# Kernel optimization log

Hardware: AMD Instinct MI355X
Metric: run time of the kernel (lower is better)

Reference implementation:

```python
import jax, jax.numpy as jnp
import numpy as np

N = 50000          # nodes
E = 800000         # edges (avg degree 16)
FEATS = [96, 96, 96, 48]


def setup_inputs() -> dict:
    key = jax.random.key(0)
    ks = jax.random.split(key, 10)
    x = jax.random.normal(ks[0], (N, FEATS[0]), dtype=jnp.float32)
    edge_index = jax.random.randint(ks[1], (2, E), 0, N, dtype=jnp.int64)
    d = {"x": x, "edge_index": edge_index}
    i = 2
    for l in range(3):
        s = 1.0 / np.sqrt(FEATS[l])
        d[f"Wl{l}"] = jax.random.uniform(ks[i], (FEATS[l], FEATS[l + 1]), jnp.float32, -s, s); i += 1
        d[f"Wr{l}"] = jax.random.uniform(ks[i], (FEATS[l], FEATS[l + 1]), jnp.float32, -s, s); i += 1
        d[f"b{l}"] = jnp.zeros((FEATS[l + 1],), jnp.float32)
    return d


def _sage_layer(h, src, dst, Wl, Wr, b, n):
    # PyG SAGEConv (aggr='mean', root_weight=True, normalize=False):
    # out_i = W_l @ mean_{j in N(i)} h_j + W_r @ h_i + b
    msg = h[src]                                                   # [E, F] gather
    ssum = jax.ops.segment_sum(msg, dst, num_segments=n)           # [N, F] scatter-add
    cnt = jax.ops.segment_sum(jnp.ones((src.shape[0], 1), h.dtype), dst, num_segments=n)
    mean = ssum / jnp.maximum(cnt, 1.0)
    return mean @ Wl + h @ Wr + b


def reference(x, edge_index, Wl0, Wr0, b0, Wl1, Wr1, b1, Wl2, Wr2, b2):
    src, dst = edge_index[0], edge_index[1]
    n = x.shape[0]
    # block = SAGEConv -> ReLU -> dropout(identity in eval)
    h = jax.nn.relu(_sage_layer(x, src, dst, Wl0, Wr0, b0, n))
    h = jax.nn.relu(_sage_layer(h, src, dst, Wl1, Wr1, b1, n))
    h = jax.nn.relu(_sage_layer(h, src, dst, Wl2, Wr2, b2, n))
    return h
```

## Files before the change

### kernel.cpp

```cpp
#include <hip/hip_runtime.h>


#define NNODES 50000
#define ZROW   50000
#define NEDGES 800000
#define CAP    64
#define LSTR   72
#define NBKT   512
#define BKSZ   98
#define NBKB   511
#define EBA    400
#define EPBA   2000
#define SEGC   20
#define CVT_N8 600000
#define CB 1172
#define WTN 46080
#define WB 90

typedef __attribute__((ext_vector_type(8))) short bf16x8;
typedef __attribute__((ext_vector_type(4))) float f32x4;

__device__ inline unsigned short f2bf(float f) {
    unsigned int u = __float_as_uint(f);
    unsigned int r = (u + 0x7fffu + ((u >> 16) & 1u)) >> 16;
    return (unsigned short)r;
}
__device__ inline float bf2f_lo(unsigned int u) { return __uint_as_float(u << 16); }
__device__ inline float bf2f_hi(unsigned int u) { return __uint_as_float(u & 0xffff0000u); }

__global__ __launch_bounds__(512) void build_a(
        const int* __restrict__ src, const int* __restrict__ dst,
        unsigned int* __restrict__ region, unsigned char* __restrict__ cnta,
        const float* __restrict__ x, unsigned short* __restrict__ h0b,
        const float* __restrict__ Wl0, const float* __restrict__ Wr0,
        const float* __restrict__ Wl1, const float* __restrict__ Wr1,
        const float* __restrict__ Wl2, const float* __restrict__ Wr2,
        unsigned short* __restrict__ WT0, unsigned short* __restrict__ WT1,
        unsigned short* __restrict__ WT2l, unsigned short* __restrict__ WT2r) {
    int b = blockIdx.x;
    if (b < EBA) {
        __shared__ int hist[NBKT];
        const int t = threadIdx.x;
        for (int k = t; k < NBKT; k += 512) hist[k] = 0;
        __syncthreads();
        const int e0 = b * EPBA;
        for (int i = t; i < EPBA; i += 512) {
            int d = dst[e0 + i];
            int s = src[e0 + i];
            unsigned int bk = (unsigned int)d / 98u;
            unsigned int rel = (unsigned int)d - bk * 98u;
            unsigned int val = (rel << 16) | (unsigned int)s;
            int r = atomicAdd(&hist[bk], 1);
            if (r < SEGC) region[((size_t)b * NBKT + bk) * SEGC + r] = val;
        }
        __syncthreads();
        for (int k = t; k < NBKT; k += 512)
            cnta[(size_t)k * EBA + b] = (unsigned char)min(hist[k], SEGC);
    } else if (b < EBA + CB) {
        long long t = (long long)(b - EBA) * 512 + threadIdx.x;
        if (t < CVT_N8) {
            const float4* p = reinterpret_cast<const float4*>(x + t * 8);
            float4 a = p[0], c = p[1];
            uint4 o;
            o.x = (unsigned)f2bf(a.x) | ((unsigned)f2bf(a.y) << 16);
            o.y = (unsigned)f2bf(a.z) | ((unsigned)f2bf(a.w) << 16);
            o.z = (unsigned)f2bf(c.x) | ((unsigned)f2bf(c.y) << 16);
            o.w = (unsigned)f2bf(c.z) | ((unsigned)f2bf(c.w) << 16);
            *reinterpret_cast<uint4*>(h0b + t * 8) = o;
        }
    } else if (b < EBA + CB + WB) {
        int t = (b - EBA - CB) * 512 + threadIdx.x;
        if (t >= WTN) return;
        if (t < 18432) {
            int u = t; int j = u / 192; int k = u - j * 192;
            float v = (k < 96) ? Wl0[k * 96 + j] : Wr0[(k - 96) * 96 + j];
            WT0[u] = f2bf(v);
        } else if (t < 36864) {
            int u = t - 18432; int j = u / 192; int k = u - j * 192;
            float v = (k < 96) ? Wl1[k * 96 + j] : Wr1[(k - 96) * 96 + j];
            WT1[u] = f2bf(v);
        } else if (t < 41472) {
            int u = t - 36864; int j = u / 96; int k = u - j * 96;
            WT2l[u] = f2bf(Wl2[k * 48 + j]);
        } else {
            int u = t - 41472; int j = u / 96; int k = u - j * 96;
            WT2r[u] = f2bf(Wr2[k * 48 + j]);
        }
    } else {
        int t = threadIdx.x;
        if (t < 12) {
            uint4 z = make_uint4(0, 0, 0, 0);
            *reinterpret_cast<uint4*>(h0b + (size_t)ZROW * 96 + t * 8) = z;
        }
    }
}

__global__ __launch_bounds__(512) void build_b(const unsigned int* __restrict__ region,
                                               const unsigned char* __restrict__ cnta,
                                               int* __restrict__ deg,
                                               unsigned short* __restrict__ colu) {
    __shared__ unsigned char cnt_l[EBA];
    __shared__ int deg_l[BKSZ];
    __shared__ __attribute__((aligned(16))) unsigned short colu_l[BKSZ * CAP];
    const int k = blockIdx.x;
    const int t = threadIdx.x;
    const int base_node = k * BKSZ;
    const int nn = min(BKSZ, NNODES - base_node);
    for (int i = t; i < EBA; i += 512) cnt_l[i] = cnta[(size_t)k * EBA + i];
    if (t < BKSZ) deg_l[t] = 0;
    __syncthreads();

    for (int cb = t; cb < EBA; cb += 512) {
        const int c = cnt_l[cb];
        const unsigned int* cell = region + ((size_t)cb * NBKT + k) * SEGC;
        for (int j = 0; j < c; j += 4) {
            uint4 q = *reinterpret_cast<const uint4*>(cell + j);
            unsigned int qq0 = q.x, qq1 = q.y, qq2 = q.z, qq3 = q.w;
            if (j + 0 < c) {
                int local = (int)(qq0 >> 16);
                int r = atomicAdd(&deg_l[local], 1);
                if (r < CAP) colu_l[local * CAP + r] = (unsigned short)(qq0 & 0xffffu);
            }
            if (j + 1 < c) {
                int local = (int)(qq1 >> 16);
                int r = atomicAdd(&deg_l[local], 1);
                if (r < CAP) colu_l[local * CAP + r] = (unsigned short)(qq1 & 0xffffu);
            }
            if (j + 2 < c) {
                int local = (int)(qq2 >> 16);
                int r = atomicAdd(&deg_l[local], 1);
                if (r < CAP) colu_l[local * CAP + r] = (unsigned short)(qq2 & 0xffffu);
            }
            if (j + 3 < c) {
                int local = (int)(qq3 >> 16);
                int r = atomicAdd(&deg_l[local], 1);
                if (r < CAP) colu_l[local * CAP + r] = (unsigned short)(qq3 & 0xffffu);
            }
        }
    }
    __syncthreads();

    for (int i = t; i < nn * (CAP / 8); i += 512) {
        *reinterpret_cast<uint4*>(colu + (size_t)base_node * CAP + i * 8) =
            *reinterpret_cast<const uint4*>(colu_l + i * 8);
    }
    if (t < nn) deg[base_node + t] = deg_l[t];
}

template <int NT, bool Y2EP>
__global__ __launch_bounds__(256) void fused_layer(
    const unsigned short* __restrict__ hb,
    const int* __restrict__ deg, const unsigned short* __restrict__ colu,
    const unsigned short* __restrict__ WT,
    const float* __restrict__ bias,
    unsigned short* __restrict__ out_bf,
    const unsigned short* __restrict__ WT2l,
    unsigned short* __restrict__ Y2b) {
    __shared__ unsigned short Asm[16][200];
    __shared__ unsigned short cols[16 * LSTR];
    const int i0 = blockIdx.x * 16;
    const int t = threadIdx.x;

    if (blockIdx.x == 0) {
        if (t < 12) {
            uint4 z = make_uint4(0, 0, 0, 0);
            *reinterpret_cast<uint4*>(out_bf + (size_t)ZROW * 96 + t * 8) = z;
        }
        if (Y2EP && t >= 16 && t < 22) {
            uint4 z = make_uint4(0, 0, 0, 0);
            *reinterpret_cast<uint4*>(Y2b + (size_t)ZROW * 48 + (t - 16) * 8) = z;
        }
    }

    {
        int u4 = t * 4;
        int node = u4 >> 6;
        int slot = u4 & 63;
        uint2 v = *reinterpret_cast<const uint2*>(colu + (size_t)(i0 + node) * CAP + slot);
        int d = deg[i0 + node];
        unsigned int s0 = (slot + 0 < d) ? (v.x & 0xffffu) : ZROW;
        unsigned int s1 = (slot + 1 < d) ? (v.x >> 16)     : ZROW;
        unsigned int s2 = (slot + 2 < d) ? (v.y & 0xffffu) : ZROW;
        unsigned int s3 = (slot + 3 < d) ? (v.y >> 16)     : ZROW;
        uint2 o;
        o.x = s0 | (s1 << 16);
        o.y = s2 | (s3 << 16);
        *reinterpret_cast<uint2*>(&cols[node * LSTR + slot]) = o;
    }
    __syncthreads();

    if (t < 192) {
        const int nl = t / 12;
        const int c = (t - nl * 12) * 8;
        const int d = deg[i0 + nl];
        const int d8 = d & ~7;
        const int pd4 = (d + 3) & ~3;
        float a0 = 0.f, a1 = 0.f, a2 = 0.f, a3 = 0.f, a4 = 0.f, a5 = 0.f, a6 = 0.f, a7 = 0.f;
        int j = 0;
        for (; j < d8; j += 8) {
            uint4 cu = *reinterpret_cast<const uint4*>(&cols[nl * LSTR + j]);
            int s0 = (int)(cu.x & 0xffffu), s1 = (int)(cu.x >> 16);
            int s2 = (int)(cu.y & 0xffffu), s3 = (int)(cu.y >> 16);
            int s4 = (int)(cu.z & 0xffffu), s5 = (int)(cu.z >> 16);
            int s6 = (int)(cu.w & 0xffffu), s7 = (int)(cu.w >> 16);
            uint4 u0 = *reinterpret_cast<const uint4*>(hb + (size_t)s0 * 96 + c);
            uint4 u1 = *reinterpret_cast<const uint4*>(hb + (size_t)s1 * 96 + c);
            uint4 u2 = *reinterpret_cast<const uint4*>(hb + (size_t)s2 * 96 + c);
            uint4 u3 = *reinterpret_cast<const uint4*>(hb + (size_t)s3 * 96 + c);
            uint4 u4 = *reinterpret_cast<const uint4*>(hb + (size_t)s4 * 96 + c);
            uint4 u5 = *reinterpret_cast<const uint4*>(hb + (size_t)s5 * 96 + c);
            uint4 u6 = *reinterpret_cast<const uint4*>(hb + (size_t)s6 * 96 + c);
            uint4 u7 = *reinterpret_cast<const uint4*>(hb + (size_t)s7 * 96 + c);
            a0 += bf2f_lo(u0.x) + bf2f_lo(u1.x) + bf2f_lo(u2.x) + bf2f_lo(u3.x)
                + bf2f_lo(u4.x) + bf2f_lo(u5.x) + bf2f_lo(u6.x) + bf2f_lo(u7.x);
            a1 += bf2f_hi(u0.x) + bf2f_hi(u1.x) + bf2f_hi(u2.x) + bf2f_hi(u3.x)
                + bf2f_hi(u4.x) + bf2f_hi(u5.x) + bf2f_hi(u6.x) + bf2f_hi(u7.x);
            a2 += bf2f_lo(u0.y) + bf2f_lo(u1.y) + bf2f_lo(u2.y) + bf2f_lo(u3.y)
                + bf2f_lo(u4.y) + bf2f_lo(u5.y) + bf2f_lo(u6.y) + bf2f_lo(u7.y);
            a3 += bf2f_hi(u0.y) + bf2f_hi(u1.y) + bf2f_hi(u2.y) + bf2f_hi(u3.y)
                + bf2f_hi(u4.y) + bf2f_hi(u5.y) + bf2f_hi(u6.y) + bf2f_hi(u7.y);
            a4 += bf2f_lo(u0.z) + bf2f_lo(u1.z) + bf2f_lo(u2.z) + bf2f_lo(u3.z)
                + bf2f_lo(u4.z) + bf2f_lo(u5.z) + bf2f_lo(u6.z) + bf2f_lo(u7.z);
            a5 += bf2f_hi(u0.z) + bf2f_hi(u1.z) + bf2f_hi(u2.z) + bf2f_hi(u3.z)
                + bf2f_hi(u4.z) + bf2f_hi(u5.z) + bf2f_hi(u6.z) + bf2f_hi(u7.z);
            a6 += bf2f_lo(u0.w) + bf2f_lo(u1.w) + bf2f_lo(u2.w) + bf2f_lo(u3.w)
                + bf2f_lo(u4.w) + bf2f_lo(u5.w) + bf2f_lo(u6.w) + bf2f_lo(u7.w);
            a7 += bf2f_hi(u0.w) + bf2f_hi(u1.w) + bf2f_hi(u2.w) + bf2f_hi(u3.w)
                + bf2f_hi(u4.w) + bf2f_hi(u5.w) + bf2f_hi(u6.w) + bf2f_hi(u7.w);
        }
        for (; j < pd4; j += 4) {
            uint2 cu = *reinterpret_cast<const uint2*>(&cols[nl * LSTR + j]);
            int s0 = (int)(cu.x & 0xffffu), s1 = (int)(cu.x >> 16);
            int s2 = (int)(cu.y & 0xffffu), s3 = (int)(cu.y >> 16);
            uint4 u0 = *reinterpret_cast<const uint4*>(hb + (size_t)s0 * 96 + c);
            uint4 u1 = *reinterpret_cast<const uint4*>(hb + (size_t)s1 * 96 + c);
            uint4 u2 = *reinterpret_cast<const uint4*>(hb + (size_t)s2 * 96 + c);
            uint4 u3 = *reinterpret_cast<const uint4*>(hb + (size_t)s3 * 96 + c);
            a0 += bf2f_lo(u0.x) + bf2f_lo(u1.x) + bf2f_lo(u2.x) + bf2f_lo(u3.x);
            a1 += bf2f_hi(u0.x) + bf2f_hi(u1.x) + bf2f_hi(u2.x) + bf2f_hi(u3.x);
            a2 += bf2f_lo(u0.y) + bf2f_lo(u1.y) + bf2f_lo(u2.y) + bf2f_lo(u3.y);
            a3 += bf2f_hi(u0.y) + bf2f_hi(u1.y) + bf2f_hi(u2.y) + bf2f_hi(u3.y);
            a4 += bf2f_lo(u0.z) + bf2f_lo(u1.z) + bf2f_lo(u2.z) + bf2f_lo(u3.z);
            a5 += bf2f_hi(u0.z) + bf2f_hi(u1.z) + bf2f_hi(u2.z) + bf2f_hi(u3.z);
            a6 += bf2f_lo(u0.w) + bf2f_lo(u1.w) + bf2f_lo(u2.w) + bf2f_lo(u3.w);
            a7 += bf2f_hi(u0.w) + bf2f_hi(u1.w) + bf2f_hi(u2.w) + bf2f_hi(u3.w);
        }
        float inv = (d > 0) ? 1.0f / (float)d : 0.0f;
        uint4 o;
        o.x = (unsigned)f2bf(a0 * inv) | ((unsigned)f2bf(a1 * inv) << 16);
        o.y = (unsigned)f2bf(a2 * inv) | ((unsigned)f2bf(a3 * inv) << 16);
        o.z = (unsigned)f2bf(a4 * inv) | ((unsigned)f2bf(a5 * inv) << 16);
        o.w = (unsigned)f2bf(a6 * inv) | ((unsigned)f2bf(a7 * inv) << 16);
        *reinterpret_cast<uint4*>(&Asm[nl][c]) = o;
    }
    __syncthreads();

    const int wave = t >> 6;
    const int lane = t & 63;
    const int m = lane & 15;
    const int kq = (lane >> 4) * 8;

    bf16x8 afr[6];
#pragma unroll
    for (int kk = 0; kk < 3; ++kk)
        afr[kk] = *reinterpret_cast<const bf16x8*>(&Asm[m][kq + kk * 32]);
    const unsigned short* hrow = hb + (size_t)(i0 + m) * 96 + kq;
#pragma unroll
    for (int kk = 0; kk < 3; ++kk)
        afr[3 + kk] = *reinterpret_cast<const bf16x8*>(hrow + kk * 32);

    if (Y2EP) __syncthreads();

    const int r0 = (lane >> 4) * 4;
    for (int nt = wave; nt < NT; nt += 4) {
        f32x4 acc = {0.f, 0.f, 0.f, 0.f};
        const unsigned short* wrow = WT + (size_t)(nt * 16 + m) * 192 + kq;
#pragma unroll
        for (int kk = 0; kk < 6; ++kk) {
            bf16x8 bfr = *reinterpret_cast<const bf16x8*>(wrow + kk * 32);
            acc = __builtin_amdgcn_mfma_f32_16x16x32_bf16(afr[kk], bfr, acc, 0, 0, 0);
        }
        int colj = nt * 16 + m;
        float bv = bias[colj];
#pragma unroll
        for (int r = 0; r < 4; ++r) {
            float v = fmaxf(acc[r] + bv, 0.0f);
            unsigned short hv = f2bf(v);
            out_bf[(size_t)(i0 + r0 + r) * (16 * NT) + colj] = hv;
            if (Y2EP) Asm[r0 + r][colj] = hv;
        }
    }

    if (Y2EP) {
        __syncthreads();
        if (wave < 3) {
            bf16x8 a2[3];
#pragma unroll
            for (int kk = 0; kk < 3; ++kk)
                a2[kk] = *reinterpret_cast<const bf16x8*>(&Asm[m][kq + kk * 32]);
            f32x4 acc = {0.f, 0.f, 0.f, 0.f};
            const unsigned short* wrow = WT2l + (size_t)(wave * 16 + m) * 96 + kq;
#pragma unroll
            for (int kk = 0; kk < 3; ++kk) {
                bf16x8 bfr = *reinterpret_cast<const bf16x8*>(wrow + kk * 32);
                acc = __builtin_amdgcn_mfma_f32_16x16x32_bf16(a2[kk], bfr, acc, 0, 0, 0);
            }
            int colj2 = wave * 16 + m;
#pragma unroll
            for (int r = 0; r < 4; ++r)
                Y2b[(size_t)(i0 + r0 + r) * 48 + colj2] = f2bf(acc[r]);
        }
    }
}

__global__ __launch_bounds__(256) void fused_final(
    const unsigned short* __restrict__ hb,
    const unsigned short* __restrict__ Y2b,
    const int* __restrict__ deg, const unsigned short* __restrict__ colu,
    const unsigned short* __restrict__ WT2r,
    const float* __restrict__ bias,
    float* __restrict__ out_f) {
    __shared__ float Msm[32][56];
    __shared__ unsigned short cols[32 * LSTR];
    const int i0 = blockIdx.x * 32;
    const int t = threadIdx.x;
    const int nn = min(32, NNODES - i0);

    {
        int node = t >> 3;
        int slot = (t & 7) * 8;
        uint4 v = *reinterpret_cast<const uint4*>(colu + (size_t)(i0 + node) * CAP + slot);
        int d = (node < nn) ? deg[i0 + node] : 0;
        unsigned int s0 = (slot + 0 < d) ? (v.x & 0xffffu) : ZROW;
        unsigned int s1 = (slot + 1 < d) ? (v.x >> 16)     : ZROW;
        unsigned int s2 = (slot + 2 < d) ? (v.y & 0xffffu) : ZROW;
        unsigned int s3 = (slot + 3 < d) ? (v.y >> 16)     : ZROW;
        unsigned int s4 = (slot + 4 < d) ? (v.z & 0xffffu) : ZROW;
        unsigned int s5 = (slot + 5 < d) ? (v.z >> 16)     : ZROW;
        unsigned int s6 = (slot + 6 < d) ? (v.w & 0xffffu) : ZROW;
        unsigned int s7 = (slot + 7 < d) ? (v.w >> 16)     : ZROW;
        uint4 o;
        o.x = s0 | (s1 << 16);
        o.y = s2 | (s3 << 16);
        o.z = s4 | (s5 << 16);
        o.w = s6 | (s7 << 16);
        *reinterpret_cast<uint4*>(&cols[node * LSTR + slot]) = o;
    }
    __syncthreads();

    if (t < 192) {
        const int nl = t / 6;
        const int c = (t - nl * 6) * 8;
        const int d = (nl < nn) ? deg[i0 + nl] : 0;
        const int d8 = d & ~7;
        const int pd4 = (d + 3) & ~3;
        float a0 = 0.f, a1 = 0.f, a2 = 0.f, a3 = 0.f, a4 = 0.f, a5 = 0.f, a6 = 0.f, a7 = 0.f;
        int j = 0;
        for (; j < d8; j += 8) {
            uint4 cu = *reinterpret_cast<const uint4*>(&cols[nl * LSTR + j]);
            int s0 = (int)(cu.x & 0xffffu), s1 = (int)(cu.x >> 16);
            int s2 = (int)(cu.y & 0xffffu), s3 = (int)(cu.y >> 16);
            int s4 = (int)(cu.z & 0xffffu), s5 = (int)(cu.z >> 16);
            int s6 = (int)(cu.w & 0xffffu), s7 = (int)(cu.w >> 16);
            uint4 u0 = *reinterpret_cast<const uint4*>(Y2b + (size_t)s0 * 48 + c);
            uint4 u1 = *reinterpret_cast<const uint4*>(Y2b + (size_t)s1 * 48 + c);
            uint4 u2 = *reinterpret_cast<const uint4*>(Y2b + (size_t)s2 * 48 + c);
            uint4 u3 = *reinterpret_cast<const uint4*>(Y2b + (size_t)s3 * 48 + c);
            uint4 u4 = *reinterpret_cast<const uint4*>(Y2b + (size_t)s4 * 48 + c);
            uint4 u5 = *reinterpret_cast<const uint4*>(Y2b + (size_t)s5 * 48 + c);
            uint4 u6 = *reinterpret_cast<const uint4*>(Y2b + (size_t)s6 * 48 + c);
            uint4 u7 = *reinterpret_cast<const uint4*>(Y2b + (size_t)s7 * 48 + c);
            a0 += bf2f_lo(u0.x) + bf2f_lo(u1.x) + bf2f_lo(u2.x) + bf2f_lo(u3.x)
                + bf2f_lo(u4.x) + bf2f_lo(u5.x) + bf2f_lo(u6.x) + bf2f_lo(u7.x);
            a1 += bf2f_hi(u0.x) + bf2f_hi(u1.x) + bf2f_hi(u2.x) + bf2f_hi(u3.x)
                + bf2f_hi(u4.x) + bf2f_hi(u5.x) + bf2f_hi(u6.x) + bf2f_hi(u7.x);
            a2 += bf2f_lo(u0.y) + bf2f_lo(u1.y) + bf2f_lo(u2.y) + bf2f_lo(u3.y)
                + bf2f_lo(u4.y) + bf2f_lo(u5.y) + bf2f_lo(u6.y) + bf2f_lo(u7.y);
            a3 += bf2f_hi(u0.y) + bf2f_hi(u1.y) + bf2f_hi(u2.y) + bf2f_hi(u3.y)
                + bf2f_hi(u4.y) + bf2f_hi(u5.y) + bf2f_hi(u6.y) + bf2f_hi(u7.y);
            a4 += bf2f_lo(u0.z) + bf2f_lo(u1.z) + bf2f_lo(u2.z) + bf2f_lo(u3.z)
                + bf2f_lo(u4.z) + bf2f_lo(u5.z) + bf2f_lo(u6.z) + bf2f_lo(u7.z);
            a5 += bf2f_hi(u0.z) + bf2f_hi(u1.z) + bf2f_hi(u2.z) + bf2f_hi(u3.z)
                + bf2f_hi(u4.z) + bf2f_hi(u5.z) + bf2f_hi(u6.z) + bf2f_hi(u7.z);
            a6 += bf2f_lo(u0.w) + bf2f_lo(u1.w) + bf2f_lo(u2.w) + bf2f_lo(u3.w)
                + bf2f_lo(u4.w) + bf2f_lo(u5.w) + bf2f_lo(u6.w) + bf2f_lo(u7.w);
            a7 += bf2f_hi(u0.w) + bf2f_hi(u1.w) + bf2f_hi(u2.w) + bf2f_hi(u3.w)
                + bf2f_hi(u4.w) + bf2f_hi(u5.w) + bf2f_hi(u6.w) + bf2f_hi(u7.w);
        }
        for (; j < pd4; j += 4) {
            uint2 cu = *reinterpret_cast<const uint2*>(&cols[nl * LSTR + j]);
            int s0 = (int)(cu.x & 0xffffu), s1 = (int)(cu.x >> 16);
            int s2 = (int)(cu.y & 0xffffu), s3 = (int)(cu.y >> 16);
            uint4 u0 = *reinterpret_cast<const uint4*>(Y2b + (size_t)s0 * 48 + c);
            uint4 u1 = *reinterpret_cast<const uint4*>(Y2b + (size_t)s1 * 48 + c);
            uint4 u2 = *reinterpret_cast<const uint4*>(Y2b + (size_t)s2 * 48 + c);
            uint4 u3 = *reinterpret_cast<const uint4*>(Y2b + (size_t)s3 * 48 + c);
            a0 += bf2f_lo(u0.x) + bf2f_lo(u1.x) + bf2f_lo(u2.x) + bf2f_lo(u3.x);
            a1 += bf2f_hi(u0.x) + bf2f_hi(u1.x) + bf2f_hi(u2.x) + bf2f_hi(u3.x);
            a2 += bf2f_lo(u0.y) + bf2f_lo(u1.y) + bf2f_lo(u2.y) + bf2f_lo(u3.y);
            a3 += bf2f_hi(u0.y) + bf2f_hi(u1.y) + bf2f_hi(u2.y) + bf2f_hi(u3.y);
            a4 += bf2f_lo(u0.z) + bf2f_lo(u1.z) + bf2f_lo(u2.z) + bf2f_lo(u3.z);
            a5 += bf2f_hi(u0.z) + bf2f_hi(u1.z) + bf2f_hi(u2.z) + bf2f_hi(u3.z);
            a6 += bf2f_lo(u0.w) + bf2f_lo(u1.w) + bf2f_lo(u2.w) + bf2f_lo(u3.w);
            a7 += bf2f_hi(u0.w) + bf2f_hi(u1.w) + bf2f_hi(u2.w) + bf2f_hi(u3.w);
        }
        float inv = (d > 0) ? 1.0f / (float)d : 0.0f;
        float4 o0 = make_float4(a0 * inv, a1 * inv, a2 * inv, a3 * inv);
        float4 o1 = make_float4(a4 * inv, a5 * inv, a6 * inv, a7 * inv);
        *reinterpret_cast<float4*>(&Msm[nl][c]) = o0;
        *reinterpret_cast<float4*>(&Msm[nl][c + 4]) = o1;
    }
    __syncthreads();

    const int wave = t >> 6;
    const int lane = t & 63;
    const int m = lane & 15;
    const int kq = (lane >> 4) * 8;
    const int r0 = (lane >> 4) * 4;

    for (int tt = wave; tt < 6; tt += 4) {
        const int rt = tt / 3;
        const int ct = tt - rt * 3;
        bf16x8 afr[3];
        const unsigned short* hrow = hb + (size_t)(i0 + rt * 16 + m) * 96 + kq;
#pragma unroll
        for (int kk = 0; kk < 3; ++kk)
            afr[kk] = *reinterpret_cast<const bf16x8*>(hrow + kk * 32);
        f32x4 acc = {0.f, 0.f, 0.f, 0.f};
        const unsigned short* wrow = WT2r + (size_t)(ct * 16 + m) * 96 + kq;
#pragma unroll
        for (int kk = 0; kk < 3; ++kk) {
            bf16x8 bfr = *reinterpret_cast<const bf16x8*>(wrow + kk * 32);
            acc = __builtin_amdgcn_mfma_f32_16x16x32_bf16(afr[kk], bfr, acc, 0, 0, 0);
        }
        int colj = ct * 16 + m;
        float bv = bias[colj];
#pragma unroll
        for (int r = 0; r < 4; ++r) {
            int row = rt * 16 + r0 + r;
            if (i0 + row < NNODES) {
                float v = fmaxf(acc[r] + Msm[row][colj] + bv, 0.0f);
                out_f[(size_t)(i0 + row) * 48 + colj] = v;
            }
        }
    }
}

extern "C" void kernel_launch(void* const* d_in, const int* in_sizes, int n_in,
                              void* d_out, int out_size, void* d_ws, size_t ws_size,
                              hipStream_t stream) {
    const float* x   = (const float*)d_in[0];
    const int*   ei  = (const int*)d_in[1];
    const float* Wl0 = (const float*)d_in[2];
    const float* Wr0 = (const float*)d_in[3];
    const float* b0  = (const float*)d_in[4];
    const float* Wl1 = (const float*)d_in[5];
    const float* Wr1 = (const float*)d_in[6];
    const float* b1  = (const float*)d_in[7];
    const float* Wl2 = (const float*)d_in[8];
    const float* Wr2 = (const float*)d_in[9];
    const float* b2  = (const float*)d_in[10];
    float* out = (float*)d_out;

    const int* src = ei;
    const int* dst = ei + NEDGES;

    char* p = (char*)d_ws;
    int* deg = (int*)p;                        p += (size_t)50176 * 4;
    unsigned short* colu = (unsigned short*)p; p += (size_t)50176 * CAP * 2;
    unsigned char* cnta = (unsigned char*)p;   p += (size_t)NBKT * EBA;
    unsigned short* WT0 = (unsigned short*)p;  p += 96 * 192 * 2;
    unsigned short* WT1 = (unsigned short*)p;  p += 96 * 192 * 2;
    unsigned short* WT2l = (unsigned short*)p; p += 48 * 96 * 2;
    unsigned short* WT2r = (unsigned short*)p; p += 48 * 96 * 2;
    unsigned short* h0b = (unsigned short*)p;  p += (size_t)(NNODES + 1) * 96 * 2 + 64;
    unsigned short* h1b = (unsigned short*)p;  p += (size_t)(NNODES + 1) * 96 * 2 + 64;
    unsigned short* h2b = (unsigned short*)p;  p += (size_t)(NNODES + 1) * 96 * 2 + 64;
    unsigned short* Y2b = (unsigned short*)p;  p += (size_t)(NNODES + 1) * 48 * 2 + 64;

    unsigned int* region = (unsigned int*)h1b;

    build_a<<<EBA + CB + WB + 1, 512, 0, stream>>>(
        src, dst, region, cnta, x, h0b,
        Wl0, Wr0, Wl1, Wr1, Wl2, Wr2, WT0, WT1, WT2l, WT2r);

    build_b<<<NBKB, 512, 0, stream>>>(region, cnta, deg, colu);

    const int LB = NNODES / 16;
    const int FB = (NNODES + 31) / 32;
    fused_layer<6, false><<<LB, 256, 0, stream>>>(h0b, deg, colu, WT0, b0, h1b,
                                                  nullptr, nullptr);
    fused_layer<6, true><<<LB, 256, 0, stream>>>(h1b, deg, colu, WT1, b1, h2b,
                                                 WT2l, Y2b);
    fused_final<<<FB, 256, 0, stream>>>(h2b, Y2b, deg, colu, WT2r, b2, out);
}
```

Baseline: 191.9 us.

## Fuse all stages into one cooperative persistent kernel with grid syncs

Replaces five separate launches (two graph build passes, two SAGE layers, final layer) with a single cooperative kernel of 512 blocks that runs each phase in turn, separated by grid-wide syncs. The layer phases use atomic tile counters for dynamic work distribution. Tiles grow from 16 to 32 rows (64 in the final layer) with 512 threads per block. The aim is to remove inter-kernel launch gaps and tail effects, at the cost of grid-sync overhead, lower occupancy constraints and a shared-memory footprint that is the union of all phases. A fallback to separate launches is kept in case the cooperative launch fails.

```diff
diff --git a/kernel.cpp b/kernel.cpp
--- a/kernel.cpp
+++ b/kernel.cpp
@@ -1,4 +1,7 @@
 #include <hip/hip_runtime.h>
+#include <hip/hip_cooperative_groups.h>
+
+namespace cg = cooperative_groups;
 
 
 #define NNODES 50000
@@ -9,13 +12,14 @@
 #define NBKT   512
 #define BKSZ   98
 #define NBKB   511
-#define EBA    400
-#define EPBA   2000
+#define EBA    512
+#define EPBA   1563
 #define SEGC   20
 #define CVT_N8 600000
-#define CB 1172
-#define WTN 46080
-#define WB 90
+#define WTN    46080
+#define NTILE_L 1563
+#define NTILE_F 782
+#define HROWS  50016
 
 typedef __attribute__((ext_vector_type(8))) short bf16x8;
 typedef __attribute__((ext_vector_type(4))) float f32x4;
@@ -28,91 +32,95 @@
 __device__ inline float bf2f_lo(unsigned int u) { return __uint_as_float(u << 16); }
 __device__ inline float bf2f_hi(unsigned int u) { return __uint_as_float(u & 0xffff0000u); }
 
-__global__ __launch_bounds__(512) void build_a(
-        const int* __restrict__ src, const int* __restrict__ dst,
-        unsigned int* __restrict__ region, unsigned char* __restrict__ cnta,
-        const float* __restrict__ x, unsigned short* __restrict__ h0b,
-        const float* __restrict__ Wl0, const float* __restrict__ Wr0,
-        const float* __restrict__ Wl1, const float* __restrict__ Wr1,
-        const float* __restrict__ Wl2, const float* __restrict__ Wr2,
-        unsigned short* __restrict__ WT0, unsigned short* __restrict__ WT1,
-        unsigned short* __restrict__ WT2l, unsigned short* __restrict__ WT2r) {
-    int b = blockIdx.x;
-    if (b < EBA) {
-        __shared__ int hist[NBKT];
-        const int t = threadIdx.x;
-        for (int k = t; k < NBKT; k += 512) hist[k] = 0;
-        __syncthreads();
-        const int e0 = b * EPBA;
-        for (int i = t; i < EPBA; i += 512) {
-            int d = dst[e0 + i];
-            int s = src[e0 + i];
-            unsigned int bk = (unsigned int)d / 98u;
-            unsigned int rel = (unsigned int)d - bk * 98u;
-            unsigned int val = (rel << 16) | (unsigned int)s;
-            int r = atomicAdd(&hist[bk], 1);
-            if (r < SEGC) region[((size_t)b * NBKT + bk) * SEGC + r] = val;
-        }
-        __syncthreads();
-        for (int k = t; k < NBKT; k += 512)
-            cnta[(size_t)k * EBA + b] = (unsigned char)min(hist[k], SEGC);
-    } else if (b < EBA + CB) {
-        long long t = (long long)(b - EBA) * 512 + threadIdx.x;
-        if (t < CVT_N8) {
-            const float4* p = reinterpret_cast<const float4*>(x + t * 8);
-            float4 a = p[0], c = p[1];
-            uint4 o;
-            o.x = (unsigned)f2bf(a.x) | ((unsigned)f2bf(a.y) << 16);
-            o.y = (unsigned)f2bf(a.z) | ((unsigned)f2bf(a.w) << 16);
-            o.z = (unsigned)f2bf(c.x) | ((unsigned)f2bf(c.y) << 16);
-            o.w = (unsigned)f2bf(c.z) | ((unsigned)f2bf(c.w) << 16);
-            *reinterpret_cast<uint4*>(h0b + t * 8) = o;
-        }
-    } else if (b < EBA + CB + WB) {
-        int t = (b - EBA - CB) * 512 + threadIdx.x;
-        if (t >= WTN) return;
-        if (t < 18432) {
-            int u = t; int j = u / 192; int k = u - j * 192;
-            float v = (k < 96) ? Wl0[k * 96 + j] : Wr0[(k - 96) * 96 + j];
-            WT0[u] = f2bf(v);
-        } else if (t < 36864) {
-            int u = t - 18432; int j = u / 192; int k = u - j * 192;
-            float v = (k < 96) ? Wl1[k * 96 + j] : Wr1[(k - 96) * 96 + j];
-            WT1[u] = f2bf(v);
-        } else if (t < 41472) {
-            int u = t - 36864; int j = u / 96; int k = u - j * 96;
-            WT2l[u] = f2bf(Wl2[k * 48 + j]);
-        } else {
-            int u = t - 41472; int j = u / 96; int k = u - j * 96;
-            WT2r[u] = f2bf(Wr2[k * 48 + j]);
-        }
-    } else {
-        int t = threadIdx.x;
-        if (t < 12) {
-            uint4 z = make_uint4(0, 0, 0, 0);
-            *reinterpret_cast<uint4*>(h0b + (size_t)ZROW * 96 + t * 8) = z;
-        }
-    }
-}
-
-__global__ __launch_bounds__(512) void build_b(const unsigned int* __restrict__ region,
-                                               const unsigned char* __restrict__ cnta,
-                                               int* __restrict__ deg,
-                                               unsigned short* __restrict__ colu) {
+struct Params {
+    const int* src; const int* dst; const float* x;
+    int* deg; unsigned short* colu; unsigned char* cnta; unsigned int* region;
+    unsigned short* WT0; unsigned short* WT1;
+    unsigned short* WT2l; unsigned short* WT2r;
+    unsigned short* h0b; unsigned short* h1b; unsigned short* h2b;
+    unsigned short* Y2b;
+    int* ctrs;
+    const float* Wl0; const float* Wr0; const float* b0;
+    const float* Wl1; const float* Wr1; const float* b1;
+    const float* Wl2; const float* Wr2; const float* b2;
+    float* out;
+};
+
+__device__ void phaseA(const Params& p, int b, int t) {
+    __shared__ int hist[NBKT];
+    for (int k = t; k < NBKT; k += 512) hist[k] = 0;
+    __syncthreads();
+    const int e0 = b * EPBA;
+    const int eN = min(e0 + EPBA, NEDGES);
+    for (int e = e0 + t; e < eN; e += 512) {
+        int d = p.dst[e];
+        int s = p.src[e];
+        unsigned int bk = (unsigned int)d / 98u;
+        unsigned int rel = (unsigned int)d - bk * 98u;
+        unsigned int val = (rel << 16) | (unsigned int)s;
+        int r = atomicAdd(&hist[bk], 1);
+        if (r < SEGC) p.region[((size_t)b * NBKT + bk) * SEGC + r] = val;
+    }
+    __syncthreads();
+    for (int k = t; k < NBKT; k += 512)
+        p.cnta[(size_t)k * EBA + b] = (unsigned char)min(hist[k], SEGC);
+
+    for (long long i = (long long)b * 512 + t; i < CVT_N8; i += (long long)EBA * 512) {
+        const float4* pp = reinterpret_cast<const float4*>(p.x + i * 8);
+        float4 a = pp[0], c = pp[1];
+        uint4 o;
+        o.x = (unsigned)f2bf(a.x) | ((unsigned)f2bf(a.y) << 16);
+        o.y = (unsigned)f2bf(a.z) | ((unsigned)f2bf(a.w) << 16);
+        o.z = (unsigned)f2bf(c.x) | ((unsigned)f2bf(c.y) << 16);
+        o.w = (unsigned)f2bf(c.z) | ((unsigned)f2bf(c.w) << 16);
+        *reinterpret_cast<uint4*>(p.h0b + i * 8) = o;
+    }
+    {
+        int u = b * 512 + t;
+        if (u < 18432) {
+            int j = u / 192, k = u - j * 192;
+            float v = (k < 96) ? p.Wl0[k * 96 + j] : p.Wr0[(k - 96) * 96 + j];
+            p.WT0[u] = f2bf(v);
+        } else if (u < 36864) {
+            int w = u - 18432; int j = w / 192, k = w - j * 192;
+            float v = (k < 96) ? p.Wl1[k * 96 + j] : p.Wr1[(k - 96) * 96 + j];
+            p.WT1[w] = f2bf(v);
+        } else if (u < 41472) {
+            int w = u - 36864; int j = w / 96, k = w - j * 96;
+            p.WT2l[w] = f2bf(p.Wl2[k * 48 + j]);
+        } else if (u < WTN) {
+            int w = u - 41472; int j = w / 96, k = w - j * 96;
+            p.WT2r[w] = f2bf(p.Wr2[k * 48 + j]);
+        }
+    }
+    if (b == 0) {
+        uint4 z = make_uint4(0, 0, 0, 0);
+        if (t < 12)
+            *reinterpret_cast<uint4*>(p.h0b + (size_t)ZROW * 96 + t * 8) = z;
+        else if (t >= 16 && t < 28)
+            *reinterpret_cast<uint4*>(p.h1b + (size_t)ZROW * 96 + (t - 16) * 8) = z;
+        else if (t >= 32 && t < 44)
+            *reinterpret_cast<uint4*>(p.h2b + (size_t)ZROW * 96 + (t - 32) * 8) = z;
+        else if (t >= 48 && t < 54)
+            *reinterpret_cast<uint4*>(p.Y2b + (size_t)ZROW * 48 + (t - 48) * 8) = z;
+        else if (t >= 60 && t < 64)
+            p.ctrs[t - 60] = 0;
+    }
+}
+
+__device__ void phaseB(const Params& p, int k, int t) {
     __shared__ unsigned char cnt_l[EBA];
     __shared__ int deg_l[BKSZ];
     __shared__ __attribute__((aligned(16))) unsigned short colu_l[BKSZ * CAP];
-    const int k = blockIdx.x;
-    const int t = threadIdx.x;
     const int base_node = k * BKSZ;
     const int nn = min(BKSZ, NNODES - base_node);
-    for (int i = t; i < EBA; i += 512) cnt_l[i] = cnta[(size_t)k * EBA + i];
+    cnt_l[t] = p.cnta[(size_t)k * EBA + t];
     if (t < BKSZ) deg_l[t] = 0;
     __syncthreads();
 
-    for (int cb = t; cb < EBA; cb += 512) {
-        const int c = cnt_l[cb];
-        const unsigned int* cell = region + ((size_t)cb * NBKT + k) * SEGC;
+    {
+        const int c = cnt_l[t];
+        const unsigned int* cell = p.region + ((size_t)t * NBKT + k) * SEGC;
         for (int j = 0; j < c; j += 4) {
             uint4 q = *reinterpret_cast<const uint4*>(cell + j);
             unsigned int qq0 = q.x, qq1 = q.y, qq2 = q.z, qq3 = q.w;
@@ -141,64 +149,54 @@
     __syncthreads();
 
     for (int i = t; i < nn * (CAP / 8); i += 512) {
-        *reinterpret_cast<uint4*>(colu + (size_t)base_node * CAP + i * 8) =
+        *reinterpret_cast<uint4*>(p.colu + (size_t)base_node * CAP + i * 8) =
             *reinterpret_cast<const uint4*>(colu_l + i * 8);
     }
-    if (t < nn) deg[base_node + t] = deg_l[t];
+    if (t < nn) p.deg[base_node + t] = deg_l[t];
 }
 
 template <int NT, bool Y2EP>
-__global__ __launch_bounds__(256) void fused_layer(
-    const unsigned short* __restrict__ hb,
-    const int* __restrict__ deg, const unsigned short* __restrict__ colu,
-    const unsigned short* __restrict__ WT,
-    const float* __restrict__ bias,
-    unsigned short* __restrict__ out_bf,
-    const unsigned short* __restrict__ WT2l,
-    unsigned short* __restrict__ Y2b) {
-    __shared__ unsigned short Asm[16][200];
-    __shared__ unsigned short cols[16 * LSTR];
-    const int i0 = blockIdx.x * 16;
-    const int t = threadIdx.x;
-
-    if (blockIdx.x == 0) {
-        if (t < 12) {
-            uint4 z = make_uint4(0, 0, 0, 0);
-            *reinterpret_cast<uint4*>(out_bf + (size_t)ZROW * 96 + t * 8) = z;
-        }
-        if (Y2EP && t >= 16 && t < 22) {
-            uint4 z = make_uint4(0, 0, 0, 0);
-            *reinterpret_cast<uint4*>(Y2b + (size_t)ZROW * 48 + (t - 16) * 8) = z;
-        }
-    }
-
-    {
-        int u4 = t * 4;
-        int node = u4 >> 6;
-        int slot = u4 & 63;
-        uint2 v = *reinterpret_cast<const uint2*>(colu + (size_t)(i0 + node) * CAP + slot);
-        int d = deg[i0 + node];
+__device__ void layerTile(const Params& p, int i0, int t,
+                          const unsigned short* __restrict__ hb,
+                          const unsigned short* __restrict__ WT,
+                          const float* __restrict__ bias,
+                          unsigned short* __restrict__ out_bf) {
+    __shared__ unsigned short colsL[32 * LSTR];
+    __shared__ unsigned short AsmL[32][200];
+    const int nn = min(32, NNODES - i0);
+
+    if (t < 256) {
+        int node = t >> 3;
+        int slot = (t & 7) * 8;
+        uint4 v = *reinterpret_cast<const uint4*>(p.colu + (size_t)(i0 + node) * CAP + slot);
+        int d = (node < nn) ? p.deg[i0 + node] : 0;
         unsigned int s0 = (slot + 0 < d) ? (v.x & 0xffffu) : ZROW;
         unsigned int s1 = (slot + 1 < d) ? (v.x >> 16)     : ZROW;
         unsigned int s2 = (slot + 2 < d) ? (v.y & 0xffffu) : ZROW;
         unsigned int s3 = (slot + 3 < d) ? (v.y >> 16)     : ZROW;
-        uint2 o;
+        unsigned int s4 = (slot + 4 < d) ? (v.z & 0xffffu) : ZROW;
+        unsigned int s5 = (slot + 5 < d) ? (v.z >> 16)     : ZROW;
+        unsigned int s6 = (slot + 6 < d) ? (v.w & 0xffffu) : ZROW;
+        unsigned int s7 = (slot + 7 < d) ? (v.w >> 16)     : ZROW;
+        uint4 o;
         o.x = s0 | (s1 << 16);
         o.y = s2 | (s3 << 16);
-        *reinterpret_cast<uint2*>(&cols[node * LSTR + slot]) = o;
-    }
-    __syncthreads();
-
-    if (t < 192) {
+        o.z = s4 | (s5 << 16);
+        o.w = s6 | (s7 << 16);
+        *reinterpret_cast<uint4*>(&colsL[node * LSTR + slot]) = o;
+    }
+    __syncthreads();
+
+    if (t < 384) {
         const int nl = t / 12;
         const int c = (t - nl * 12) * 8;
-        const int d = deg[i0 + nl];
+        const int d = (nl < nn) ? p.deg[i0 + nl] : 0;
         const int d8 = d & ~7;
         const int pd4 = (d + 3) & ~3;
         float a0 = 0.f, a1 = 0.f, a2 = 0.f, a3 = 0.f, a4 = 0.f, a5 = 0.f, a6 = 0.f, a7 = 0.f;
         int j = 0;
         for (; j < d8; j += 8) {
-            uint4 cu = *reinterpret_cast<const uint4*>(&cols[nl * LSTR + j]);
+            uint4 cu = *reinterpret_cast<const uint4*>(&colsL[nl * LSTR + j]);
             int s0 = (int)(cu.x & 0xffffu), s1 = (int)(cu.x >> 16);
             int s2 = (int)(cu.y & 0xffffu), s3 = (int)(cu.y >> 16);
             int s4 = (int)(cu.z & 0xffffu), s5 = (int)(cu.z >> 16);
@@ -229,7 +227,7 @@
                 + bf2f_hi(u4.w) + bf2f_hi(u5.w) + bf2f_hi(u6.w) + bf2f_hi(u7.w);
         }
         for (; j < pd4; j += 4) {
-            uint2 cu = *reinterpret_cast<const uint2*>(&cols[nl * LSTR + j]);
+            uint2 cu = *reinterpret_cast<const uint2*>(&colsL[nl * LSTR + j]);
             int s0 = (int)(cu.x & 0xffffu), s1 = (int)(cu.x >> 16);
             int s2 = (int)(cu.y & 0xffffu), s3 = (int)(cu.y >> 16);
             uint4 u0 = *reinterpret_cast<const uint4*>(hb + (size_t)s0 * 96 + c);
@@ -251,7 +249,7 @@
         o.y = (unsigned)f2bf(a2 * inv) | ((unsigned)f2bf(a3 * inv) << 16);
         o.z = (unsigned)f2bf(a4 * inv) | ((unsigned)f2bf(a5 * inv) << 16);
         o.w = (unsigned)f2bf(a6 * inv) | ((unsigned)f2bf(a7 * inv) << 16);
-        *reinterpret_cast<uint4*>(&Asm[nl][c]) = o;
+        *reinterpret_cast<uint4*>(&AsmL[nl][c]) = o;
     }
     __syncthreads();
 
@@ -259,78 +257,85 @@
     const int lane = t & 63;
     const int m = lane & 15;
     const int kq = (lane >> 4) * 8;
-
-    bf16x8 afr[6];
-#pragma unroll
-    for (int kk = 0; kk < 3; ++kk)
-        afr[kk] = *reinterpret_cast<const bf16x8*>(&Asm[m][kq + kk * 32]);
-    const unsigned short* hrow = hb + (size_t)(i0 + m) * 96 + kq;
-#pragma unroll
-    for (int kk = 0; kk < 3; ++kk)
-        afr[3 + kk] = *reinterpret_cast<const bf16x8*>(hrow + kk * 32);
-
+    const int r0 = (lane >> 4) * 4;
+
+    bf16x8 afrA[2][3];
+#pragma unroll
+    for (int rt = 0; rt < 2; ++rt)
+#pragma unroll
+        for (int kk = 0; kk < 3; ++kk)
+            afrA[rt][kk] = *reinterpret_cast<const bf16x8*>(&AsmL[rt * 16 + m][kq + kk * 32]);
     if (Y2EP) __syncthreads();
 
-    const int r0 = (lane >> 4) * 4;
-    for (int nt = wave; nt < NT; nt += 4) {
+    for (int tt = wave; tt < 2 * NT; tt += 8) {
+        const int rt = tt / NT;
+        const int ct = tt - rt * NT;
+        bf16x8 afrB[3];
+        const unsigned short* hrow = hb + (size_t)(i0 + rt * 16 + m) * 96 + kq;
+#pragma unroll
+        for (int kk = 0; kk < 3; ++kk)
+            afrB[kk] = *reinterpret_cast<const bf16x8*>(hrow + kk * 32);
         f32x4 acc = {0.f, 0.f, 0.f, 0.f};
-        const unsigned short* wrow = WT + (size_t)(nt * 16 + m) * 192 + kq;
-#pragma unroll
-        for (int kk = 0; kk < 6; ++kk) {
+        const unsigned short* wrow = WT + (size_t)(ct * 16 + m) * 192 + kq;
+#pragma unroll
+        for (int kk = 0; kk < 3; ++kk) {
             bf16x8 bfr = *reinterpret_cast<const bf16x8*>(wrow + kk * 32);
-            acc = __builtin_amdgcn_mfma_f32_16x16x32_bf16(afr[kk], bfr, acc, 0, 0, 0);
-        }
-        int colj = nt * 16 + m;
+            acc = __builtin_amdgcn_mfma_f32_16x16x32_bf16(afrA[rt][kk], bfr, acc, 0, 0, 0);
+        }
+#pragma unroll
+        for (int kk = 0; kk < 3; ++kk) {
+            bf16x8 bfr = *reinterpret_cast<const bf16x8*>(wrow + (3 + kk) * 32);
+            acc = __builtin_amdgcn_mfma_f32_16x16x32_bf16(afrB[kk], bfr, acc, 0, 0, 0);
+        }
+        int colj = ct * 16 + m;
         float bv = bias[colj];
 #pragma unroll
         for (int r = 0; r < 4; ++r) {
+            int row = rt * 16 + r0 + r;
             float v = fmaxf(acc[r] + bv, 0.0f);
             unsigned short hv = f2bf(v);
-            out_bf[(size_t)(i0 + r0 + r) * (16 * NT) + colj] = hv;
-            if (Y2EP) Asm[r0 + r][colj] = hv;
+            if (i0 + row < NNODES)
+                out_bf[(size_t)(i0 + row) * 96 + colj] = hv;
+            if (Y2EP) AsmL[row][colj] = hv;
         }
     }
 
     if (Y2EP) {
         __syncthreads();
-        if (wave < 3) {
+        if (wave < 6) {
+            const int rt2 = wave / 3;
+            const int ct2 = wave - rt2 * 3;
             bf16x8 a2[3];
 #pragma unroll
             for (int kk = 0; kk < 3; ++kk)
-                a2[kk] = *reinterpret_cast<const bf16x8*>(&Asm[m][kq + kk * 32]);
+                a2[kk] = *reinterpret_cast<const bf16x8*>(&AsmL[rt2 * 16 + m][kq + kk * 32]);
             f32x4 acc = {0.f, 0.f, 0.f, 0.f};
-            const unsigned short* wrow = WT2l + (size_t)(wave * 16 + m) * 96 + kq;
+            const unsigned short* wrow = p.WT2l + (size_t)(ct2 * 16 + m) * 96 + kq;
 #pragma unroll
             for (int kk = 0; kk < 3; ++kk) {
                 bf16x8 bfr = *reinterpret_cast<const bf16x8*>(wrow + kk * 32);
                 acc = __builtin_amdgcn_mfma_f32_16x16x32_bf16(a2[kk], bfr, acc, 0, 0, 0);
             }
-            int colj2 = wave * 16 + m;
-#pragma unroll
-            for (int r = 0; r < 4; ++r)
-                Y2b[(size_t)(i0 + r0 + r) * 48 + colj2] = f2bf(acc[r]);
-        }
-    }
-}
-
-__global__ __launch_bounds__(256) void fused_final(
-    const unsigned short* __restrict__ hb,
-    const unsigned short* __restrict__ Y2b,
-    const int* __restrict__ deg, const unsigned short* __restrict__ colu,
-    const unsigned short* __restrict__ WT2r,
-    const float* __restrict__ bias,
-    float* __restrict__ out_f) {
-    __shared__ float Msm[32][56];
-    __shared__ unsigned short cols[32 * LSTR];
-    const int i0 = blockIdx.x * 32;
-    const int t = threadIdx.x;
-    const int nn = min(32, NNODES - i0);
+            int colj2 = ct2 * 16 + m;
+#pragma unroll
+            for (int r = 0; r < 4; ++r) {
+                int gl = i0 + rt2 * 16 + r0 + r;
+                if (gl < NNODES) p.Y2b[(size_t)gl * 48 + colj2] = f2bf(acc[r]);
+            }
+        }
+    }
+}
+
+__device__ void finalTile(const Params& p, int i0, int t) {
+    __shared__ unsigned short colsF[64 * LSTR];
+    __shared__ float MsmF[64][56];
+    const int nn = min(64, NNODES - i0);
 
     {
         int node = t >> 3;
         int slot = (t & 7) * 8;
-        uint4 v = *reinterpret_cast<const uint4*>(colu + (size_t)(i0 + node) * CAP + slot);
-        int d = (node < nn) ? deg[i0 + node] : 0;
+        uint4 v = *reinterpret_cast<const uint4*>(p.colu + (size_t)(i0 + node) * CAP + slot);
+        int d = (node < nn) ? p.deg[i0 + node] : 0;
         unsigned int s0 = (slot + 0 < d) ? (v.x & 0xffffu) : ZROW;
         unsigned int s1 = (slot + 1 < d) ? (v.x >> 16)     : ZROW;
         unsigned int s2 = (slot + 2 < d) ? (v.y & 0xffffu) : ZROW;
@@ -344,32 +349,32 @@
         o.y = s2 | (s3 << 16);
         o.z = s4 | (s5 << 16);
         o.w = s6 | (s7 << 16);
-        *reinterpret_cast<uint4*>(&cols[node * LSTR + slot]) = o;
-    }
-    __syncthreads();
-
-    if (t < 192) {
+        *reinterpret_cast<uint4*>(&colsF[node * LSTR + slot]) = o;
+    }
+    __syncthreads();
+
+    if (t < 384) {
         const int nl = t / 6;
         const int c = (t - nl * 6) * 8;
-        const int d = (nl < nn) ? deg[i0 + nl] : 0;
+        const int d = (nl < nn) ? p.deg[i0 + nl] : 0;
         const int d8 = d & ~7;
         const int pd4 = (d + 3) & ~3;
         float a0 = 0.f, a1 = 0.f, a2 = 0.f, a3 = 0.f, a4 = 0.f, a5 = 0.f, a6 = 0.f, a7 = 0.f;
         int j = 0;
         for (; j < d8; j += 8) {
-            uint4 cu = *reinterpret_cast<const uint4*>(&cols[nl * LSTR + j]);
+            uint4 cu = *reinterpret_cast<const uint4*>(&colsF[nl * LSTR + j]);
             int s0 = (int)(cu.x & 0xffffu), s1 = (int)(cu.x >> 16);
             int s2 = (int)(cu.y & 0xffffu), s3 = (int)(cu.y >> 16);
             int s4 = (int)(cu.z & 0xffffu), s5 = (int)(cu.z >> 16);
             int s6 = (int)(cu.w & 0xffffu), s7 = (int)(cu.w >> 16);
-            uint4 u0 = *reinterpret_cast<const uint4*>(Y2b + (size_t)s0 * 48 + c);
-            uint4 u1 = *reinterpret_cast<const uint4*>(Y2b + (size_t)s1 * 48 + c);
-            uint4 u2 = *reinterpret_cast<const uint4*>(Y2b + (size_t)s2 * 48 + c);
-            uint4 u3 = *reinterpret_cast<const uint4*>(Y2b + (size_t)s3 * 48 + c);
-            uint4 u4 = *reinterpret_cast<const uint4*>(Y2b + (size_t)s4 * 48 + c);
-            uint4 u5 = *reinterpret_cast<const uint4*>(Y2b + (size_t)s5 * 48 + c);
-            uint4 u6 = *reinterpret_cast<const uint4*>(Y2b + (size_t)s6 * 48 + c);
-            uint4 u7 = *reinterpret_cast<const uint4*>(Y2b + (size_t)s7 * 48 + c);
+            uint4 u0 = *reinterpret_cast<const uint4*>(p.Y2b + (size_t)s0 * 48 + c);
+            uint4 u1 = *reinterpret_cast<const uint4*>(p.Y2b + (size_t)s1 * 48 + c);
+            uint4 u2 = *reinterpret_cast<const uint4*>(p.Y2b + (size_t)s2 * 48 + c);
+            uint4 u3 = *reinterpret_cast<const uint4*>(p.Y2b + (size_t)s3 * 48 + c);
+            uint4 u4 = *reinterpret_cast<const uint4*>(p.Y2b + (size_t)s4 * 48 + c);
+            uint4 u5 = *reinterpret_cast<const uint4*>(p.Y2b + (size_t)s5 * 48 + c);
+            uint4 u6 = *reinterpret_cast<const uint4*>(p.Y2b + (size_t)s6 * 48 + c);
+            uint4 u7 = *reinterpret_cast<const uint4*>(p.Y2b + (size_t)s7 * 48 + c);
             a0 += bf2f_lo(u0.x) + bf2f_lo(u1.x) + bf2f_lo(u2.x) + bf2f_lo(u3.x)
                 + bf2f_lo(u4.x) + bf2f_lo(u5.x) + bf2f_lo(u6.x) + bf2f_lo(u7.x);
             a1 += bf2f_hi(u0.x) + bf2f_hi(u1.x) + bf2f_hi(u2.x) + bf2f_hi(u3.x)
@@ -388,13 +393,13 @@
                 + bf2f_hi(u4.w) + bf2f_hi(u5.w) + bf2f_hi(u6.w) + bf2f_hi(u7.w);
         }
         for (; j < pd4; j += 4) {
-            uint2 cu = *reinterpret_cast<const uint2*>(&cols[nl * LSTR + j]);
+            uint2 cu = *reinterpret_cast<const uint2*>(&colsF[nl * LSTR + j]);
             int s0 = (int)(cu.x & 0xffffu), s1 = (int)(cu.x >> 16);
             int s2 = (int)(cu.y & 0xffffu), s3 = (int)(cu.y >> 16);
-            uint4 u0 = *reinterpret_cast<const uint4*>(Y2b + (size_t)s0 * 48 + c);
-            uint4 u1 = *reinterpret_cast<const uint4*>(Y2b + (size_t)s1 * 48 + c);
-            uint4 u2 = *reinterpret_cast<const uint4*>(Y2b + (size_t)s2 * 48 + c);
-            uint4 u3 = *reinterpret_cast<const uint4*>(Y2b + (size_t)s3 * 48 + c);
+            uint4 u0 = *reinterpret_cast<const uint4*>(p.Y2b + (size_t)s0 * 48 + c);
+            uint4 u1 = *reinterpret_cast<const uint4*>(p.Y2b + (size_t)s1 * 48 + c);
+            uint4 u2 = *reinterpret_cast<const uint4*>(p.Y2b + (size_t)s2 * 48 + c);
+            uint4 u3 = *reinterpret_cast<const uint4*>(p.Y2b + (size_t)s3 * 48 + c);
             a0 += bf2f_lo(u0.x) + bf2f_lo(u1.x) + bf2f_lo(u2.x) + bf2f_lo(u3.x);
             a1 += bf2f_hi(u0.x) + bf2f_hi(u1.x) + bf2f_hi(u2.x) + bf2f_hi(u3.x);
             a2 += bf2f_lo(u0.y) + bf2f_lo(u1.y) + bf2f_lo(u2.y) + bf2f_lo(u3.y);
@@ -407,8 +412,8 @@
         float inv = (d > 0) ? 1.0f / (float)d : 0.0f;
         float4 o0 = make_float4(a0 * inv, a1 * inv, a2 * inv, a3 * inv);
         float4 o1 = make_float4(a4 * inv, a5 * inv, a6 * inv, a7 * inv);
-        *reinterpret_cast<float4*>(&Msm[nl][c]) = o0;
-        *reinterpret_cast<float4*>(&Msm[nl][c + 4]) = o1;
+        *reinterpret_cast<float4*>(&MsmF[nl][c]) = o0;
+        *reinterpret_cast<float4*>(&MsmF[nl][c + 4]) = o1;
     }
     __syncthreads();
 
@@ -418,79 +423,126 @@
     const int kq = (lane >> 4) * 8;
     const int r0 = (lane >> 4) * 4;
 
-    for (int tt = wave; tt < 6; tt += 4) {
+    for (int tt = wave; tt < 12; tt += 8) {
         const int rt = tt / 3;
         const int ct = tt - rt * 3;
         bf16x8 afr[3];
-        const unsigned short* hrow = hb + (size_t)(i0 + rt * 16 + m) * 96 + kq;
+        const unsigned short* hrow = p.h2b + (size_t)(i0 + rt * 16 + m) * 96 + kq;
 #pragma unroll
         for (int kk = 0; kk < 3; ++kk)
             afr[kk] = *reinterpret_cast<const bf16x8*>(hrow + kk * 32);
         f32x4 acc = {0.f, 0.f, 0.f, 0.f};
-        const unsigned short* wrow = WT2r + (size_t)(ct * 16 + m) * 96 + kq;
+        const unsigned short* wrow = p.WT2r + (size_t)(ct * 16 + m) * 96 + kq;
 #pragma unroll
         for (int kk = 0; kk < 3; ++kk) {
             bf16x8 bfr = *reinterpret_cast<const bf16x8*>(wrow + kk * 32);
             acc = __builtin_amdgcn_mfma_f32_16x16x32_bf16(afr[kk], bfr, acc, 0, 0, 0);
         }
         int colj = ct * 16 + m;
-        float bv = bias[colj];
+        float bv = p.b2[colj];
 #pragma unroll
         for (int r = 0; r < 4; ++r) {
             int row = rt * 16 + r0 + r;
             if (i0 + row < NNODES) {
-                float v = fmaxf(acc[r] + Msm[row][colj] + bv, 0.0f);
-                out_f[(size_t)(i0 + row) * 48 + colj] = v;
-            }
-        }
-    }
-}
+                float v = fmaxf(acc[r] + MsmF[row][colj] + bv, 0.0f);
+                p.out[(size_t)(i0 + row) * 48 + colj] = v;
+            }
+        }
+    }
+}
+
+__global__ __launch_bounds__(512, 4) void mega(Params p) {
+    const int b = blockIdx.x;
+    const int t = threadIdx.x;
+    cg::grid_group g = cg::this_grid();
+    __shared__ int sTile;
+
+    phaseA(p, b, t);
+    g.sync();
+    if (b < NBKB) phaseB(p, b, t);
+    g.sync();
+    for (;;) {
+        __syncthreads();
+        if (t == 0) sTile = atomicAdd(&p.ctrs[0], 1);
+        __syncthreads();
+        int tile = sTile;
+        if (tile >= NTILE_L) break;
+        layerTile<6, false>(p, tile * 32, t, p.h0b, p.WT0, p.b0, p.h1b);
+    }
+    g.sync();
+    for (;;) {
+        __syncthreads();
+        if (t == 0) sTile = atomicAdd(&p.ctrs[1], 1);
+        __syncthreads();
+        int tile = sTile;
+        if (tile >= NTILE_L) break;
+        layerTile<6, true>(p, tile * 32, t, p.h1b, p.WT1, p.b1, p.h2b);
+    }
+    g.sync();
+    for (;;) {
+        __syncthreads();
+        if (t == 0) sTile = atomicAdd(&p.ctrs[2], 1);
+        __syncthreads();
+        int tile = sTile;
+        if (tile >= NTILE_F) break;
+        finalTile(p, tile * 64, t);
+    }
+}
+
+__global__ __launch_bounds__(512) void k_buildA(Params p) { phaseA(p, blockIdx.x, threadIdx.x); }
+__global__ __launch_bounds__(512) void k_buildB(Params p) { phaseB(p, blockIdx.x, threadIdx.x); }
+__global__ __launch_bounds__(512) void k_l0(Params p) {
+    layerTile<6, false>(p, blockIdx.x * 32, threadIdx.x, p.h0b, p.WT0, p.b0, p.h1b);
+}
+__global__ __launch_bounds__(512) void k_l1(Params p) {
+    layerTile<6, true>(p, blockIdx.x * 32, threadIdx.x, p.h1b, p.WT1, p.b1, p.h2b);
+}
+__global__ __launch_bounds__(512) void k_fin(Params p) { finalTile(p, blockIdx.x * 64, threadIdx.x); }
 
 extern "C" void kernel_launch(void* const* d_in, const int* in_sizes, int n_in,
                               void* d_out, int out_size, void* d_ws, size_t ws_size,
                               hipStream_t stream) {
-    const float* x   = (const float*)d_in[0];
-    const int*   ei  = (const int*)d_in[1];
-    const float* Wl0 = (const float*)d_in[2];
-    const float* Wr0 = (const float*)d_in[3];
-    const float* b0  = (const float*)d_in[4];
-    const float* Wl1 = (const float*)d_in[5];
-    const float* Wr1 = (const float*)d_in[6];
-    const float* b1  = (const float*)d_in[7];
-    const float* Wl2 = (const float*)d_in[8];
-    const float* Wr2 = (const float*)d_in[9];
-    const float* b2  = (const float*)d_in[10];
-    float* out = (float*)d_out;
-
-    const int* src = ei;
-    const int* dst = ei + NEDGES;
-
-    char* p = (char*)d_ws;
-    int* deg = (int*)p;                        p += (size_t)50176 * 4;
-    unsigned short* colu = (unsigned short*)p; p += (size_t)50176 * CAP * 2;
-    unsigned char* cnta = (unsigned char*)p;   p += (size_t)NBKT * EBA;
-    unsigned short* WT0 = (unsigned short*)p;  p += 96 * 192 * 2;
-    unsigned short* WT1 = (unsigned short*)p;  p += 96 * 192 * 2;
-    unsigned short* WT2l = (unsigned short*)p; p += 48 * 96 * 2;
-    unsigned short* WT2r = (unsigned short*)p; p += 48 * 96 * 2;
-    unsigned short* h0b = (unsigned short*)p;  p += (size_t)(NNODES + 1) * 96 * 2 + 64;
-    unsigned short* h1b = (unsigned short*)p;  p += (size_t)(NNODES + 1) * 96 * 2 + 64;
-    unsigned short* h2b = (unsigned short*)p;  p += (size_t)(NNODES + 1) * 96 * 2 + 64;
-    unsigned short* Y2b = (unsigned short*)p;  p += (size_t)(NNODES + 1) * 48 * 2 + 64;
-
-    unsigned int* region = (unsigned int*)h1b;
-
-    build_a<<<EBA + CB + WB + 1, 512, 0, stream>>>(
-        src, dst, region, cnta, x, h0b,
-        Wl0, Wr0, Wl1, Wr1, Wl2, Wr2, WT0, WT1, WT2l, WT2r);
-
-    build_b<<<NBKB, 512, 0, stream>>>(region, cnta, deg, colu);
-
-    const int LB = NNODES / 16;
-    const int FB = (NNODES + 31) / 32;
-    fused_layer<6, false><<<LB, 256, 0, stream>>>(h0b, deg, colu, WT0, b0, h1b,
-                                                  nullptr, nullptr);
-    fused_layer<6, true><<<LB, 256, 0, stream>>>(h1b, deg, colu, WT1, b1, h2b,
-                                                 WT2l, Y2b);
-    fused_final<<<FB, 256, 0, stream>>>(h2b, Y2b, deg, colu, WT2r, b2, out);
-}
+    const int* ei = (const int*)d_in[1];
+
+    char* q = (char*)d_ws;
+    Params hp;
+    hp.deg = (int*)q;                         q += (size_t)50176 * 4;
+    hp.colu = (unsigned short*)q;             q += (size_t)50176 * CAP * 2;
+    hp.cnta = (unsigned char*)q;              q += (size_t)NBKT * EBA;
+    hp.region = (unsigned int*)q;             q += (size_t)EBA * NBKT * SEGC * 4;
+    hp.WT0 = (unsigned short*)q;              q += 96 * 192 * 2;
+    hp.WT1 = (unsigned short*)q;              q += 96 * 192 * 2;
+    hp.WT2l = (unsigned short*)q;             q += 48 * 96 * 2;
+    hp.WT2r = (unsigned short*)q;             q += 48 * 96 * 2;
+    hp.h0b = (unsigned short*)q;              q += (size_t)HROWS * 96 * 2;
+    hp.h1b = (unsigned short*)q;              q += (size_t)HROWS * 96 * 2;
+    hp.h2b = (unsigned short*)q;              q += (size_t)HROWS * 96 * 2;
+    hp.Y2b = (unsigned short*)q;              q += (size_t)HROWS * 48 * 2;
+    hp.ctrs = (int*)q;                        q += 256;
+
+    hp.src = ei;
+    hp.dst = ei + NEDGES;
+    hp.x   = (const float*)d_in[0];
+    hp.Wl0 = (const float*)d_in[2];
+    hp.Wr0 = (const float*)d_in[3];
+    hp.b0  = (const float*)d_in[4];
+    hp.Wl1 = (const float*)d_in[5];
+    hp.Wr1 = (const float*)d_in[6];
+    hp.b1  = (const float*)d_in[7];
+    hp.Wl2 = (const float*)d_in[8];
+    hp.Wr2 = (const float*)d_in[9];
+    hp.b2  = (const float*)d_in[10];
+    hp.out = (float*)d_out;
+
+    void* kargs[] = {(void*)&hp};
+    hipError_t err = hipLaunchCooperativeKernel((const void*)mega, dim3(EBA), dim3(512),
+                                                kargs, 0, stream);
+    if (err != hipSuccess) {
+        (void)hipGetLastError();
+        k_buildA<<<EBA, 512, 0, stream>>>(hp);
+        k_buildB<<<NBKB, 512, 0, stream>>>(hp);
+        k_l0<<<NTILE_L, 512, 0, stream>>>(hp);
+        k_l1<<<NTILE_L, 512, 0, stream>>>(hp);
+        k_fin<<<NTILE_F, 512, 0, stream>>>(hp);
+    }
+}
```

Result: slower. 500.3 us (+160.7%).
